# Kernel tuning notes

Hardware: AMD Instinct MI355X
Metric: run time of the kernel (lower is better)

## Reference

```python
import jax, jax.numpy as jnp
import numpy as np

B, S = 512, 256          # batch, seq_len
C, H = 8, 16             # num_cells, expert hidden size
M = 20                   # memory_size (hard-coded in module)
NT = C * H               # num_trajectories = 128
ENC_IN = M * (NT + 1)    # 20*129 = 2580, memory_encode input dim
A_H = 16                 # agent LSTM hidden


def setup_inputs() -> dict:
    key = jax.random.key(0)
    ks = jax.random.split(key, 20)
    r = lambda i, shape: 0.1 * jax.random.normal(ks[i], shape, dtype=jnp.float32)
    return {
        "x": jax.random.normal(ks[0], (B, S, 1), dtype=jnp.float32),
        "pred0": jax.random.uniform(ks[1], (B, 1), dtype=jnp.float32),
        "gate0": jax.nn.softmax(jax.random.uniform(ks[2], (B, C), dtype=jnp.float32), axis=1),
        # experts: C parallel LSTM cells (input 1, hidden H) + per-cell scalar head
        "W_ih": r(3, (C, 4 * H, 1)), "W_hh": r(4, (C, 4 * H, H)),
        "b_ih": r(5, (C, 4 * H)), "b_hh": r(6, (C, 4 * H)),
        "W_o": r(7, (C, H)), "b_o": r(8, (C,)),
        # memory_encode: Linear(2580,64) ReLU Linear(64,16) ReLU
        "W1": r(9, (64, ENC_IN)), "b1": r(10, (64,)),
        "W2": r(11, (16, 64)), "b2": r(12, (16,)),
        # gate_linear: Linear(16, C) + softmax
        "Wg": r(13, (C, 16)), "bg": r(14, (C,)),
        # agent: 2 stacked LSTM cells (16 -> 16)
        "Wa_ih": r(15, (2, 4 * A_H, A_H)), "Wa_hh": r(16, (2, 4 * A_H, A_H)),
        "ba_ih": r(17, (2, 4 * A_H)), "ba_hh": r(18, (2, 4 * A_H)),
    }


def _cell(z, c):
    # PyTorch LSTMCell gate order: i, f, g, o
    i, f, g, o = jnp.split(z, 4, axis=-1)
    c2 = jax.nn.sigmoid(f) * c + jax.nn.sigmoid(i) * jnp.tanh(g)
    return jax.nn.sigmoid(o) * jnp.tanh(c2), c2


def reference(x, pred0, gate0, W_ih, W_hh, b_ih, b_hh, W_o, b_o,
              W1, b1, W2, b2, Wg, bg, Wa_ih, Wa_hh, ba_ih, ba_hh):
    mem0 = jnp.zeros((B, M, NT + 1), jnp.float32).at[:, :, -1].set(0.5)
    eh0 = jnp.zeros((B, H), jnp.float32)   # combined expert h (shared across cells)
    a0 = jnp.zeros((2, B, A_H), jnp.float32)

    def step(carry, x_t):
        mem, eh, ec, pred, gate_state, ah, ac = carry
        error = x_t - pred                                        # [B,1]
        # experts: C LSTM cells, all reading the shared combined state
        z = (jnp.einsum('bf,cgf->bcg', x_t, W_ih)
             + jnp.einsum('bh,cgh->bcg', eh, W_hh)
             + b_ih + b_hh)                                       # [B,C,4H]
        nh, nc = _cell(z, ec[:, None, :])                          # [B,C,H]
        o = jnp.einsum('bch,ch->bc', nh, W_o) + b_o               # [B,C]
        # memory_step: matmul(mstep, mem) shifts rows down by 1, row 0 <- w
        w = jnp.concatenate([nh.reshape(B, -1), error], axis=1)   # [B,NT+1]
        mem = jnp.concatenate([w[:, None, :], mem[:, :-1, :]], axis=1)
        # memory_encode MLP
        e1 = jax.nn.relu(mem.reshape(B, -1) @ W1.T + b1)
        ai = jax.nn.relu(e1 @ W2.T + b2)                           # [B,16]
        # agent: 2 stacked LSTM cells
        ah_l, ac_l, inp_l = [], [], ai
        for l in range(2):
            zl = inp_l @ Wa_ih[l].T + ba_ih[l] + ah[l] @ Wa_hh[l].T + ba_hh[l]
            hl, cl = _cell(zl, ac[l])
            ah_l.append(hl); ac_l.append(cl)
            inp_l = hl
        ah2, ac2 = jnp.stack(ah_l), jnp.stack(ac_l)
        gate = jax.nn.softmax(inp_l @ Wg.T + bg, axis=1)           # [B,C]
        # theta = clip(2.5 * mean|mem[:, :10, -1]|, 0, 1)  (relu(t)-relu(t-1))
        theta = jnp.clip(jnp.mean(jnp.abs(mem[:, :10, -1]), axis=1) * 2.5, 0.0, 1.0)[:, None]
        gate = gate * theta + gate_state * (1.0 - theta)
        eh2 = jnp.einsum('bc,bch->bh', gate, nh)                   # bmm(gate, h)
        ec2 = jnp.einsum('bc,bch->bh', gate, nc)
        pred2 = jnp.einsum('bc,bc->b', gate, o)[:, None]           # [B,1]
        return (mem, eh2, ec2, pred2, gate, ah2, ac2), pred2

    xs = jnp.swapaxes(x, 0, 1)  # [S,B,1]
    _, preds = jax.lax.scan(step, (mem0, eh0, eh0, pred0, gate0, a0, a0), xs)
    return jnp.swapaxes(preds, 0, 1)  # [B,S,1]
```

## Files before the change

kernel.cpp:

```cpp
#include <hip/hip_runtime.h>
#include <math.h>

#define S_LEN 256
#define NCELL 8
#define HID 16
#define MEM 20
#define NB 4
#define NTHR 512
#define RSTR 2592

typedef _Float16 v8h __attribute__((ext_vector_type(8)));
typedef float v4f __attribute__((ext_vector_type(4)));

__device__ __forceinline__ float sigm(float v) { return 1.0f / (1.0f + __expf(-v)); }
__device__ __forceinline__ float tanh_f(float v) { return 1.0f - 2.0f / (__expf(2.0f * v) + 1.0f); }
__device__ __forceinline__ float dot4(float4 a, float4 b) {
    return fmaf(a.x, b.x, fmaf(a.y, b.y, fmaf(a.z, b.z, a.w * b.w)));
}
__device__ __forceinline__ v4f mfma16(v8h a, v8h b, v4f c) {
    return __builtin_amdgcn_mfma_f32_16x16x32_f16(a, b, c, 0, 0, 0);
}

#define RING(b, s, k) ringH[(b) * RSTR + (s) * 128 + (k)]

__global__ __launch_bounds__(256)
void prep_w(const float* __restrict__ W1, const float* __restrict__ W_hh,
            const float* __restrict__ W_ih, const float* __restrict__ b_ih,
            const float* __restrict__ b_hh, _Float16* __restrict__ W1F,
            _Float16* __restrict__ WAF) {
    int idx = blockIdx.x * 256 + threadIdx.x;
    if (idx < 163840) {
        int e = idx & 7, lane = (idx >> 3) & 63, jt = (idx >> 9) & 3, t = idx >> 11;
        int m = t >> 2, kc = t & 3;
        int j = jt * 16 + (lane & 15);
        int k = kc * 32 + (lane >> 4) * 8 + e;
        W1F[idx] = (_Float16)W1[j * 2580 + m * 129 + k];
    } else if (idx < 163840 + 16384) {
        int d = idx - 163840;
        int e = d & 7, lane = (d >> 3) & 63, gate = (d >> 9) & 3, c = d >> 11;
        int m = lane & 15, k = (lane >> 4) * 8 + e;
        int row = c * 64 + gate * 16 + m;
        float v = 0.f;
        if (k < 16) v = W_hh[row * 16 + k];
        else if (k == 16) v = W_ih[row];
        else if (k == 17) v = b_ih[row] + b_hh[row];
        WAF[d] = (_Float16)v;
    }
}

#define E1P(BB, V) { \
    V = b1_l[lane] \
      + red[par][1][BB][lane] + red[par][2][BB][lane] + red[par][3][BB][lane] \
      + red[par][4][BB][lane] + red[par][5][BB][lane] + red[par][6][BB][lane] \
      + red[par][7][BB][lane]; }

#define E1F(BB, V) { \
    V += errdotS[BB][lane] \
       + red0[0][BB][lane] + red0[1][BB][lane] + red0[2][BB][lane] + red0[3][BB][lane]; \
    e1S[BB][lane] = fmaxf(V, 0.f); }

__global__ __attribute__((amdgpu_flat_work_group_size(NTHR, NTHR)))
void mmoe_kernel(const float* __restrict__ x, const float* __restrict__ pred0,
                 const float* __restrict__ gate0,
                 const float* __restrict__ W_ih, const float* __restrict__ W_hh,
                 const float* __restrict__ b_ih, const float* __restrict__ b_hh,
                 const float* __restrict__ W_o, const float* __restrict__ b_o,
                 const float* __restrict__ W1, const float* __restrict__ b1,
                 const float* __restrict__ W2, const float* __restrict__ b2,
                 const float* __restrict__ Wg, const float* __restrict__ bg,
                 const float* __restrict__ Wa_ih, const float* __restrict__ Wa_hh,
                 const float* __restrict__ ba_ih, const float* __restrict__ ba_hh,
                 const _Float16* __restrict__ W1F, const _Float16* __restrict__ WAF,
                 float* __restrict__ out)
{
    __shared__ __align__(16) _Float16 ringH[NB * RSTR];
    __shared__ __align__(16) _Float16 W10F_l[8192];
    __shared__ __align__(16) _Float16 ehH[NB][40];
    __shared__ float errS[NB][MEM];
    __shared__ __align__(16) float WaI[2][64 * 20], WaH[2][64 * 20];
    __shared__ float ba_l[2][64];
    __shared__ __align__(16) float W2_l[16 * 68];
    __shared__ float b2_l[16];
    __shared__ __align__(16) float Wg_l[8][16], Wo_l[8][16];
    __shared__ float bg_l[8], bo_l[8];
    __shared__ float Werr_l[MEM * 64];
    __shared__ float b1_l[64];
    __shared__ float xS[NB][S_LEN];
    __shared__ __align__(16) float ecS[NB][HID];
    __shared__ __align__(16) float nhS[NB][NCELL][HID], ncS[NB][NCELL][HID];
    __shared__ float oS[NB][NCELL], predS[NB], gateS[NB][NCELL];
    __shared__ __align__(16) float ahS[2][NB][HID], acS[2][NB][HID];
    __shared__ __align__(16) float e1S[NB][64], aiS[NB][HID];
    __shared__ __align__(16) float glog[NB][8];
    __shared__ __align__(16) float red[2][8][NB][64];
    __shared__ __align__(16) float red0[4][NB][64];
    __shared__ float errdotS[NB][64];
    __shared__ float thS[NB];

    const int tid = threadIdx.x;
    const int b0 = blockIdx.x * NB;
    const int lane = tid & 63, wv = tid >> 6;
    const int quad = lane >> 4, nn = lane & 15, bb4 = nn & 3;

    for (int i = tid; i < 2048; i += NTHR) {
        int l = i >> 10, r = i & 1023, g = r >> 4, q = r & 15;
        WaI[l][g * 20 + q] = Wa_ih[i]; WaH[l][g * 20 + q] = Wa_hh[i];
    }
    for (int i = tid; i < 128; i += NTHR) { int l = i >> 6, g = i & 63; ba_l[l][g] = ba_ih[i] + ba_hh[i]; }
    for (int i = tid; i < 1024; i += NTHR) { int r = i >> 6, q = i & 63; W2_l[r * 68 + q] = W2[i]; }
    for (int i = tid; i < 1280; i += NTHR) { int m = i >> 6, j = i & 63; Werr_l[i] = W1[j * 2580 + m * 129 + 128]; }
    for (int i = tid; i < 8192; i += NTHR) W10F_l[i] = W1F[i];
    if (tid < 64) b1_l[tid] = b1[tid];
    if (tid < 16) b2_l[tid] = b2[tid];
    if (tid < 128) { int c = tid >> 4, h = tid & 15; Wg_l[c][h] = Wg[tid]; Wo_l[c][h] = W_o[tid]; }
    if (tid < 8) { bg_l[tid] = bg[tid]; bo_l[tid] = b_o[tid]; }
    for (int i = tid; i < NB * S_LEN; i += NTHR) { int b = i >> 8, s = i & 255; xS[b][s] = x[(b0 + b) * S_LEN + s]; }
    for (int i = tid; i < NB * RSTR; i += NTHR) ringH[i] = (_Float16)0.0f;
    for (int i = tid; i < 2 * 8 * NB * 64; i += NTHR) ((float*)red)[i] = 0.0f;
    if (tid < NB * 40) {
        int n = tid / 40, k = tid % 40;
        float v = 0.f;
        if (k == 16) v = x[(b0 + n) * S_LEN + 0];
        else if (k == 17) v = 1.0f;
        ehH[n][k] = (_Float16)v;
    }
    if (tid < NB * MEM) { int b = tid / MEM, m = tid % MEM; errS[b][m] = 0.5f; }
    if (tid < NB * HID) {
        int b = tid >> 4, h = tid & 15;
        ecS[b][h] = 0.f;
        ahS[0][b][h] = 0.f; ahS[1][b][h] = 0.f;
        acS[0][b][h] = 0.f; acS[1][b][h] = 0.f;
    }
    if (tid < NB) predS[tid] = pred0[b0 + tid];
    if (tid < NB * NCELL) { int b = tid >> 3, c = tid & 7; gateS[b][c] = gate0[(b0 + b) * NCELL + c]; }

    const v8h* WA = (const v8h*)WAF;
    v8h aI = WA[(wv * 4 + 0) * 64 + lane];
    v8h aF = WA[(wv * 4 + 1) * 64 + lane];
    v8h aG = WA[(wv * 4 + 2) * 64 + lane];
    v8h aO = WA[(wv * 4 + 3) * 64 + lane];
    __syncthreads();

    const v8h* Wb = (const v8h*)W1F;
    const v8h* WL = (const v8h*)W10F_l;

    int head = 0;
    #pragma unroll 1
    for (int t = 0; t < S_LEN; ++t) {
        head = (head == 0) ? (MEM - 1) : (head - 1);
        const int par = t & 1, np = par ^ 1;
        float v0, v1, v2, v3;

        {
            v8h bfrag = *(const v8h*)&ehH[bb4][quad * 8];
            v4f z4 = {0.f, 0.f, 0.f, 0.f};
            v4f zi = mfma16(aI, bfrag, z4);
            v4f zf = mfma16(aF, bfrag, z4);
            v4f zg = mfma16(aG, bfrag, z4);
            v4f zo = mfma16(aO, bfrag, z4);
            if (nn < 4) {
                int b = nn, c = wv;
                #pragma unroll
                for (int r = 0; r < 4; ++r) {
                    int h = quad * 4 + r;
                    float cc = ecS[b][h];
                    float c2 = sigm(zf[r]) * cc + sigm(zi[r]) * tanh_f(zg[r]);
                    float hv = sigm(zo[r]) * tanh_f(c2);
                    nhS[b][c][h] = hv; ncS[b][c][h] = c2;
                    RING(b, head, c * 16 + h) = (_Float16)hv;
                }
            }
            if (tid < NB) errS[tid][head] = xS[tid][t] - predS[tid];
        }
        __syncthreads();

        {
            int kc = wv >> 1, jt0 = (wv & 1) * 2;
            v8h bfrag = *(const v8h*)&RING(bb4, head, kc * 32 + quad * 8);
            v8h a0 = WL[(kc * 4 + jt0) * 64 + lane];
            v8h a1 = WL[(kc * 4 + jt0 + 1) * 64 + lane];
            v4f z = {0.f, 0.f, 0.f, 0.f};
            v4f c0 = mfma16(a0, bfrag, z);
            v4f c1 = mfma16(a1, bfrag, z);
            if (nn < 4) {
                *(v4f*)&red0[kc][nn][jt0 * 16 + quad * 4] = c0;
                *(v4f*)&red0[kc][nn][(jt0 + 1) * 16 + quad * 4] = c1;
            }
            if (wv == 0) {
                E1P(0, v0) E1P(1, v1) E1P(2, v2) E1P(3, v3)
            } else if (wv == 1) {
                if (lane < 32) {
                    int bb = lane >> 3, c = lane & 7;
                    const float4* np_ = (const float4*)&nhS[bb][c][0];
                    const float4* wp = (const float4*)&Wo_l[c][0];
                    float s = bo_l[c];
                    #pragma unroll
                    for (int q4 = 0; q4 < 4; ++q4) s += dot4(np_[q4], wp[q4]);
                    oS[bb][c] = s;
                }
            } else if (wv == 2) {
                if (lane < NB) {
                    float th = 0.f;
                    #pragma unroll
                    for (int m = 0; m < 10; ++m) {
                        int sl = head + m; if (sl >= MEM) sl -= MEM;
                        th += fabsf(errS[lane][sl]);
                    }
                    th *= 0.25f;
                    thS[lane] = fminf(fmaxf(th, 0.f), 1.f);
                }
            } else if (wv >= 3 && wv < 7) {
                int bb = wv - 3;
                float s = 0.f;
                int sl = head;
                #pragma unroll
                for (int m = 0; m < MEM; ++m) {
                    s = fmaf(Werr_l[m * 64 + lane], errS[bb][sl], s);
                    ++sl; if (sl >= MEM) sl = 0;
                }
                errdotS[bb][lane] = s;
            }
        }
        __syncthreads();

        if (wv >= 1) {
            int kt = (wv - 1) * 11;
            int ktEnd = kt + 11; if (ktEnd > 76) ktEnd = 76;
            v4f c0 = {0.f,0.f,0.f,0.f}, c1 = {0.f,0.f,0.f,0.f};
            v4f c2 = {0.f,0.f,0.f,0.f}, c3 = {0.f,0.f,0.f,0.f};
            size_t tb = (size_t)(4 + kt) * 256 + lane;
            v8h pA0 = Wb[tb], pA1 = Wb[tb + 64], pA2 = Wb[tb + 128], pA3 = Wb[tb + 192];
            int m0 = 1 + (kt >> 2), kc0 = kt & 3;
            int s0 = head + m0 - 1; if (s0 >= MEM) s0 -= MEM;
            v8h pB = *(const v8h*)&RING(bb4, s0, kc0 * 32 + quad * 8);
            #pragma unroll 1
            for (; kt < ktEnd; ++kt) {
                v8h A0 = pA0, A1 = pA1, A2 = pA2, A3 = pA3, B = pB;
                int kn = kt + 1;
                if (kn < ktEnd) {
                    size_t tn = (size_t)(4 + kn) * 256 + lane;
                    pA0 = Wb[tn]; pA1 = Wb[tn + 64]; pA2 = Wb[tn + 128]; pA3 = Wb[tn + 192];
                    int mn = 1 + (kn >> 2), kcn = kn & 3;
                    int sn = head + mn - 1; if (sn >= MEM) sn -= MEM;
                    pB = *(const v8h*)&RING(bb4, sn, kcn * 32 + quad * 8);
                }
                c0 = mfma16(A0, B, c0);
                c1 = mfma16(A1, B, c1);
                c2 = mfma16(A2, B, c2);
                c3 = mfma16(A3, B, c3);
            }
            if (nn < 4) {
                *(v4f*)&red[np][wv][nn][ 0 + quad * 4] = c0;
                *(v4f*)&red[np][wv][nn][16 + quad * 4] = c1;
                *(v4f*)&red[np][wv][nn][32 + quad * 4] = c2;
                *(v4f*)&red[np][wv][nn][48 + quad * 4] = c3;
            }
        } else {
            E1F(0, v0) E1F(1, v1) E1F(2, v2) E1F(3, v3)
            const int j = lane;
            {
                int bb = j >> 4, i = j & 15;
                const float4* epq = (const float4*)&e1S[bb][0];
                float s = b2_l[i];
                #pragma unroll
                for (int q = 0; q < 16; ++q) s += dot4(*(const float4*)&W2_l[i * 68 + q * 4], epq[q]);
                aiS[bb][i] = fmaxf(s, 0.f);
            }
            #pragma unroll
            for (int l = 0; l < 2; ++l) {
                int bb = j >> 4, h = j & 15;
                const float4* ip = (l == 0) ? (const float4*)&aiS[bb][0]
                                            : (const float4*)&ahS[0][bb][0];
                const float4* hp = (const float4*)&ahS[l][bb][0];
                float4 i0 = ip[0], i1 = ip[1], i2 = ip[2], i3 = ip[3];
                float4 h0 = hp[0], h1 = hp[1], h2v = hp[2], h3 = hp[3];
                float zg[4];
                #pragma unroll
                for (int gi = 0; gi < 4; ++gi) {
                    int g = gi * 16 + h;
                    const float* wi = &WaI[l][g * 20];
                    const float* wh = &WaH[l][g * 20];
                    float z = ba_l[l][g];
                    z += dot4(i0, *(const float4*)&wi[0]) + dot4(i1, *(const float4*)&wi[4])
                       + dot4(i2, *(const float4*)&wi[8]) + dot4(i3, *(const float4*)&wi[12]);
                    z += dot4(h0, *(const float4*)&wh[0]) + dot4(h1, *(const float4*)&wh[4])
                       + dot4(h2v, *(const float4*)&wh[8]) + dot4(h3, *(const float4*)&wh[12]);
                    zg[gi] = z;
                }
                float c2 = sigm(zg[1]) * acS[l][bb][h] + sigm(zg[0]) * tanh_f(zg[2]);
                acS[l][bb][h] = c2;
                ahS[l][bb][h] = sigm(zg[3]) * tanh_f(c2);
            }
            if (j < 32) {
                int bb = j >> 3, c = j & 7;
                const float4* hp = (const float4*)&ahS[1][bb][0];
                const float4* wg = (const float4*)&Wg_l[c][0];
                float s = bg_l[c];
                #pragma unroll
                for (int q = 0; q < 4; ++q) s += dot4(wg[q], hp[q]);
                glog[bb][c] = s;
                float4 ga = *(const float4*)&glog[bb][0];
                float4 gb = *(const float4*)&glog[bb][4];
                float mx = fmaxf(fmaxf(fmaxf(ga.x, ga.y), fmaxf(ga.z, ga.w)),
                                 fmaxf(fmaxf(gb.x, gb.y), fmaxf(gb.z, gb.w)));
                float sum = __expf(ga.x - mx) + __expf(ga.y - mx) + __expf(ga.z - mx) + __expf(ga.w - mx)
                          + __expf(gb.x - mx) + __expf(gb.y - mx) + __expf(gb.z - mx) + __expf(gb.w - mx);
                float p = __expf(s - mx) / sum;
                float th = thS[bb];
                gateS[bb][c] = p * th + gateS[bb][c] * (1.f - th);
            }
            {
                int bb = j >> 4, h = j & 15;
                float se = 0.f, sc = 0.f;
                #pragma unroll
                for (int c = 0; c < 8; ++c) {
                    float g = gateS[bb][c];
                    se = fmaf(g, nhS[bb][c][h], se);
                    sc = fmaf(g, ncS[bb][c][h], sc);
                }
                ehH[bb][h] = (_Float16)se;
                ecS[bb][h] = sc;
            }
            if (j < NB) {
                float s = 0.f;
                #pragma unroll
                for (int c = 0; c < 8; ++c) s = fmaf(gateS[j][c], oS[j][c], s);
                predS[j] = s;
                out[(b0 + j) * S_LEN + t] = s;
                ehH[j][16] = (_Float16)((t + 1 < S_LEN) ? xS[j][t + 1] : 0.f);
            }
        }
        __syncthreads();
    }
}

extern "C" void kernel_launch(void* const* d_in, const int* in_sizes, int n_in,
                              void* d_out, int out_size, void* d_ws, size_t ws_size,
                              hipStream_t stream) {
    const float* xp    = (const float*)d_in[0];
    const float* pred0 = (const float*)d_in[1];
    const float* gate0 = (const float*)d_in[2];
    const float* W_ih  = (const float*)d_in[3];
    const float* W_hh  = (const float*)d_in[4];
    const float* b_ih  = (const float*)d_in[5];
    const float* b_hh  = (const float*)d_in[6];
    const float* W_o   = (const float*)d_in[7];
    const float* b_o   = (const float*)d_in[8];
    const float* W1    = (const float*)d_in[9];
    const float* b1    = (const float*)d_in[10];
    const float* W2    = (const float*)d_in[11];
    const float* b2    = (const float*)d_in[12];
    const float* Wg    = (const float*)d_in[13];
    const float* bg    = (const float*)d_in[14];
    const float* Wa_ih = (const float*)d_in[15];
    const float* Wa_hh = (const float*)d_in[16];
    const float* ba_ih = (const float*)d_in[17];
    const float* ba_hh = (const float*)d_in[18];
    _Float16* W1F = (_Float16*)d_ws;
    _Float16* WAF = W1F + 163840;

    prep_w<<<(163840 + 16384 + 255) / 256, 256, 0, stream>>>(
        W1, W_hh, W_ih, b_ih, b_hh, W1F, WAF);
    mmoe_kernel<<<512 / NB, NTHR, 0, stream>>>(
        xp, pred0, gate0, W_ih, W_hh, b_ih, b_hh, W_o, b_o,
        W1, b1, W2, b2, Wg, bg, Wa_ih, Wa_hh, ba_ih, ba_hh,
        W1F, WAF, (float*)d_out);
}
```

Measured before the change: 1.314 ms.

## Compute memory-encoder partial products for two timesteps per W1 load

The bulk W1·memory matmul over older memory slots now runs only on even steps. Each loaded W1 tile is applied to both the current ring window and the window shifted by one slot, producing partial sums for the next two timesteps. On odd steps the one slot that differs (the newest hidden state times the second W1 block) is computed from a second LDS-resident W1 copy. This halves the global W1 streaming per step, at the cost of extra LDS, doubled MFMA work on even steps and uneven per-step load.

```diff
diff --git a/kernel.cpp b/kernel.cpp
--- a/kernel.cpp
+++ b/kernel.cpp
@@ -48,11 +48,16 @@
     }
 }
 
-#define E1P(BB, V) { \
+#define E1P_ODD(BB, V) { \
     V = b1_l[lane] \
-      + red[par][1][BB][lane] + red[par][2][BB][lane] + red[par][3][BB][lane] \
-      + red[par][4][BB][lane] + red[par][5][BB][lane] + red[par][6][BB][lane] \
-      + red[par][7][BB][lane]; }
+      + redP[1][BB][lane] + redP[2][BB][lane] + redP[3][BB][lane] \
+      + redP[4][BB][lane] + redP[5][BB][lane] + redP[6][BB][lane] + redP[7][BB][lane]; }
+
+#define E1P_EVEN(BB, V) { \
+    V = b1_l[lane] \
+      + redQ[1][BB][lane] + redQ[2][BB][lane] + redQ[3][BB][lane] \
+      + redQ[4][BB][lane] + redQ[5][BB][lane] + redQ[6][BB][lane] + redQ[7][BB][lane] \
+      + redD[0][BB][lane] + redD[1][BB][lane] + redD[2][BB][lane] + redD[3][BB][lane]; }
 
 #define E1F(BB, V) { \
     V += errdotS[BB][lane] \
@@ -75,6 +80,7 @@
 {
     __shared__ __align__(16) _Float16 ringH[NB * RSTR];
     __shared__ __align__(16) _Float16 W10F_l[8192];
+    __shared__ __align__(16) _Float16 W11F_l[8192];
     __shared__ __align__(16) _Float16 ehH[NB][40];
     __shared__ float errS[NB][MEM];
     __shared__ __align__(16) float WaI[2][64 * 20], WaH[2][64 * 20];
@@ -92,7 +98,9 @@
     __shared__ __align__(16) float ahS[2][NB][HID], acS[2][NB][HID];
     __shared__ __align__(16) float e1S[NB][64], aiS[NB][HID];
     __shared__ __align__(16) float glog[NB][8];
-    __shared__ __align__(16) float red[2][8][NB][64];
+    __shared__ __align__(16) float redP[8][NB][64];
+    __shared__ __align__(16) float redQ[8][NB][64];
+    __shared__ __align__(16) float redD[4][NB][64];
     __shared__ __align__(16) float red0[4][NB][64];
     __shared__ float errdotS[NB][64];
     __shared__ float thS[NB];
@@ -109,14 +117,15 @@
     for (int i = tid; i < 128; i += NTHR) { int l = i >> 6, g = i & 63; ba_l[l][g] = ba_ih[i] + ba_hh[i]; }
     for (int i = tid; i < 1024; i += NTHR) { int r = i >> 6, q = i & 63; W2_l[r * 68 + q] = W2[i]; }
     for (int i = tid; i < 1280; i += NTHR) { int m = i >> 6, j = i & 63; Werr_l[i] = W1[j * 2580 + m * 129 + 128]; }
-    for (int i = tid; i < 8192; i += NTHR) W10F_l[i] = W1F[i];
+    for (int i = tid; i < 8192; i += NTHR) { W10F_l[i] = W1F[i]; W11F_l[i] = W1F[8192 + i]; }
     if (tid < 64) b1_l[tid] = b1[tid];
     if (tid < 16) b2_l[tid] = b2[tid];
     if (tid < 128) { int c = tid >> 4, h = tid & 15; Wg_l[c][h] = Wg[tid]; Wo_l[c][h] = W_o[tid]; }
     if (tid < 8) { bg_l[tid] = bg[tid]; bo_l[tid] = b_o[tid]; }
     for (int i = tid; i < NB * S_LEN; i += NTHR) { int b = i >> 8, s = i & 255; xS[b][s] = x[(b0 + b) * S_LEN + s]; }
     for (int i = tid; i < NB * RSTR; i += NTHR) ringH[i] = (_Float16)0.0f;
-    for (int i = tid; i < 2 * 8 * NB * 64; i += NTHR) ((float*)red)[i] = 0.0f;
+    for (int i = tid; i < 8 * NB * 64; i += NTHR) { ((float*)redP)[i] = 0.0f; ((float*)redQ)[i] = 0.0f; }
+    for (int i = tid; i < 4 * NB * 64; i += NTHR) ((float*)redD)[i] = 0.0f;
     if (tid < NB * 40) {
         int n = tid / 40, k = tid % 40;
         float v = 0.f;
@@ -142,13 +151,14 @@
     __syncthreads();
 
     const v8h* Wb = (const v8h*)W1F;
-    const v8h* WL = (const v8h*)W10F_l;
+    const v8h* WL0 = (const v8h*)W10F_l;
+    const v8h* WL1 = (const v8h*)W11F_l;
 
     int head = 0;
     #pragma unroll 1
     for (int t = 0; t < S_LEN; ++t) {
         head = (head == 0) ? (MEM - 1) : (head - 1);
-        const int par = t & 1, np = par ^ 1;
+        const int par = t & 1;
         float v0, v1, v2, v3;
 
         {
@@ -177,8 +187,8 @@
         {
             int kc = wv >> 1, jt0 = (wv & 1) * 2;
             v8h bfrag = *(const v8h*)&RING(bb4, head, kc * 32 + quad * 8);
-            v8h a0 = WL[(kc * 4 + jt0) * 64 + lane];
-            v8h a1 = WL[(kc * 4 + jt0 + 1) * 64 + lane];
+            v8h a0 = WL0[(kc * 4 + jt0) * 64 + lane];
+            v8h a1 = WL0[(kc * 4 + jt0 + 1) * 64 + lane];
             v4f z = {0.f, 0.f, 0.f, 0.f};
             v4f c0 = mfma16(a0, bfrag, z);
             v4f c1 = mfma16(a1, bfrag, z);
@@ -186,8 +196,19 @@
                 *(v4f*)&red0[kc][nn][jt0 * 16 + quad * 4] = c0;
                 *(v4f*)&red0[kc][nn][(jt0 + 1) * 16 + quad * 4] = c1;
             }
+            if (par == 1) {
+                v8h d0 = WL1[(kc * 4 + jt0) * 64 + lane];
+                v8h d1 = WL1[(kc * 4 + jt0 + 1) * 64 + lane];
+                v4f e0 = mfma16(d0, bfrag, z);
+                v4f e1 = mfma16(d1, bfrag, z);
+                if (nn < 4) {
+                    *(v4f*)&redD[kc][nn][jt0 * 16 + quad * 4] = e0;
+                    *(v4f*)&redD[kc][nn][(jt0 + 1) * 16 + quad * 4] = e1;
+                }
+            }
             if (wv == 0) {
-                E1P(0, v0) E1P(1, v1) E1P(2, v2) E1P(3, v3)
+                if (par == 0) { E1P_EVEN(0, v0) E1P_EVEN(1, v1) E1P_EVEN(2, v2) E1P_EVEN(3, v3) }
+                else         { E1P_ODD(0, v0)  E1P_ODD(1, v1)  E1P_ODD(2, v2)  E1P_ODD(3, v3) }
             } else if (wv == 1) {
                 if (lane < 32) {
                     int bb = lane >> 3, c = lane & 7;
@@ -223,39 +244,7 @@
         }
         __syncthreads();
 
-        if (wv >= 1) {
-            int kt = (wv - 1) * 11;
-            int ktEnd = kt + 11; if (ktEnd > 76) ktEnd = 76;
-            v4f c0 = {0.f,0.f,0.f,0.f}, c1 = {0.f,0.f,0.f,0.f};
-            v4f c2 = {0.f,0.f,0.f,0.f}, c3 = {0.f,0.f,0.f,0.f};
-            size_t tb = (size_t)(4 + kt) * 256 + lane;
-            v8h pA0 = Wb[tb], pA1 = Wb[tb + 64], pA2 = Wb[tb + 128], pA3 = Wb[tb + 192];
-            int m0 = 1 + (kt >> 2), kc0 = kt & 3;
-            int s0 = head + m0 - 1; if (s0 >= MEM) s0 -= MEM;
-            v8h pB = *(const v8h*)&RING(bb4, s0, kc0 * 32 + quad * 8);
-            #pragma unroll 1
-            for (; kt < ktEnd; ++kt) {
-                v8h A0 = pA0, A1 = pA1, A2 = pA2, A3 = pA3, B = pB;
-                int kn = kt + 1;
-                if (kn < ktEnd) {
-                    size_t tn = (size_t)(4 + kn) * 256 + lane;
-                    pA0 = Wb[tn]; pA1 = Wb[tn + 64]; pA2 = Wb[tn + 128]; pA3 = Wb[tn + 192];
-                    int mn = 1 + (kn >> 2), kcn = kn & 3;
-                    int sn = head + mn - 1; if (sn >= MEM) sn -= MEM;
-                    pB = *(const v8h*)&RING(bb4, sn, kcn * 32 + quad * 8);
-                }
-                c0 = mfma16(A0, B, c0);
-                c1 = mfma16(A1, B, c1);
-                c2 = mfma16(A2, B, c2);
-                c3 = mfma16(A3, B, c3);
-            }
-            if (nn < 4) {
-                *(v4f*)&red[np][wv][nn][ 0 + quad * 4] = c0;
-                *(v4f*)&red[np][wv][nn][16 + quad * 4] = c1;
-                *(v4f*)&red[np][wv][nn][32 + quad * 4] = c2;
-                *(v4f*)&red[np][wv][nn][48 + quad * 4] = c3;
-            }
-        } else {
+        if (wv == 0) {
             E1F(0, v0) E1F(1, v1) E1F(2, v2) E1F(3, v3)
             const int j = lane;
             {
@@ -328,6 +317,49 @@
                 predS[j] = s;
                 out[(b0 + j) * S_LEN + t] = s;
                 ehH[j][16] = (_Float16)((t + 1 < S_LEN) ? xS[j][t + 1] : 0.f);
+            }
+        } else if (par == 0) {
+            int kt = (wv - 1) * 11;
+            int ktEnd = kt + 11; if (ktEnd > 76) ktEnd = 76;
+            v4f c0 = {0.f,0.f,0.f,0.f}, c1 = {0.f,0.f,0.f,0.f};
+            v4f c2 = {0.f,0.f,0.f,0.f}, c3 = {0.f,0.f,0.f,0.f};
+            v4f d0 = {0.f,0.f,0.f,0.f}, d1 = {0.f,0.f,0.f,0.f};
+            v4f d2 = {0.f,0.f,0.f,0.f}, d3 = {0.f,0.f,0.f,0.f};
+            size_t tb = (size_t)(4 + kt) * 256 + lane;
+            v8h pA0 = Wb[tb], pA1 = Wb[tb + 64], pA2 = Wb[tb + 128], pA3 = Wb[tb + 192];
+            #pragma unroll 1
+            for (; kt < ktEnd; ++kt) {
+                v8h A0 = pA0, A1 = pA1, A2 = pA2, A3 = pA3;
+                int kn = kt + 1;
+                if (kn < ktEnd) {
+                    size_t tn = (size_t)(4 + kn) * 256 + lane;
+                    pA0 = Wb[tn]; pA1 = Wb[tn + 64]; pA2 = Wb[tn + 128]; pA3 = Wb[tn + 192];
+                }
+                int m = 1 + (kt >> 2), kc = kt & 3;
+                int sp = head + m - 1; if (sp >= MEM) sp -= MEM;
+                v8h BP = *(const v8h*)&RING(bb4, sp, kc * 32 + quad * 8);
+                c0 = mfma16(A0, BP, c0);
+                c1 = mfma16(A1, BP, c1);
+                c2 = mfma16(A2, BP, c2);
+                c3 = mfma16(A3, BP, c3);
+                if (m >= 2) {
+                    int sq = sp - 1; if (sq < 0) sq += MEM;
+                    v8h BQ = *(const v8h*)&RING(bb4, sq, kc * 32 + quad * 8);
+                    d0 = mfma16(A0, BQ, d0);
+                    d1 = mfma16(A1, BQ, d1);
+                    d2 = mfma16(A2, BQ, d2);
+                    d3 = mfma16(A3, BQ, d3);
+                }
+            }
+            if (nn < 4) {
+                *(v4f*)&redP[wv][nn][ 0 + quad * 4] = c0;
+                *(v4f*)&redP[wv][nn][16 + quad * 4] = c1;
+                *(v4f*)&redP[wv][nn][32 + quad * 4] = c2;
+                *(v4f*)&redP[wv][nn][48 + quad * 4] = c3;
+                *(v4f*)&redQ[wv][nn][ 0 + quad * 4] = d0;
+                *(v4f*)&redQ[wv][nn][16 + quad * 4] = d1;
+                *(v4f*)&redQ[wv][nn][32 + quad * 4] = d2;
+                *(v4f*)&redQ[wv][nn][48 + quad * 4] = d3;
             }
         }
         __syncthreads();
```

New measurement: 1.387 ms. +5.5%, slower.
